# Kernel tuning notes

Measured on AMD Instinct MI355X. Metric: run time of the kernel, lower is better.

## Reference

```python
import jax, jax.numpy as jnp
import numpy as np

R_MAX = 5.0
P_CUT = 5
NAVG = 16.0
L_OF_LM = np.array([0, 1, 1, 1, 2, 2, 2, 2, 2, 3, 3, 3, 3, 3, 3, 3])


def _sph(v):
    # real spherical harmonics up to l=3 on normalized vectors, [E,16]
    n = jnp.sqrt(jnp.sum(v * v, -1, keepdims=True) + 1e-12)
    u = v / n
    x, y, z = u[..., 0], u[..., 1], u[..., 2]
    s3, s15, s5 = np.sqrt(3.0), np.sqrt(15.0), np.sqrt(5.0)
    s70, s105, s42, s7 = np.sqrt(70.0), np.sqrt(105.0), np.sqrt(42.0), np.sqrt(7.0)
    Y = [jnp.ones_like(x),
         s3 * x, s3 * y, s3 * z,
         s15 * x * y, s15 * y * z, 0.5 * s5 * (3 * z * z - 1.0), s15 * x * z, 0.5 * s15 * (x * x - y * y),
         0.25 * s70 * y * (3 * x * x - y * y), s105 * x * y * z, 0.25 * s42 * y * (5 * z * z - 1.0),
         0.5 * s7 * z * (5 * z * z - 3.0), 0.25 * s42 * x * (5 * z * z - 1.0),
         0.5 * s105 * z * (x * x - y * y), 0.25 * s70 * x * (3 * x * x - y * y)]
    return jnp.stack(Y, -1)


def _radial(r):
    # Bessel basis * smooth polynomial cutoff, r: [E] -> [E, 8]
    n = jnp.arange(1, 9, dtype=r.dtype)
    bess = np.sqrt(2.0 / R_MAX) * jnp.sin(n * np.pi * r[:, None] / R_MAX) / (r[:, None] + 1e-9)
    u = r / R_MAX
    p = float(P_CUT)
    f = 1.0 - 0.5 * (p + 1) * (p + 2) * u ** P_CUT + p * (p + 2) * u ** (P_CUT + 1) - 0.5 * p * (p + 1) * u ** (P_CUT + 2)
    f = jnp.where(u < 1.0, f, 0.0)
    return bess * f[:, None]


def _energy(node_attrs, positions, shifts, atomic_energies, W_embed, W_up, W_r1, W_r2, W_r3,
            W_lin, W_skip, U1, U2, U3, Wc1, Wc2, Wc3, W_prod, W_readout,
            edge_index, batch, num_graphs):
    send, recv = edge_index[0], edge_index[1]
    vec = positions[recv] - positions[send] + shifts
    r = jnp.sqrt(jnp.sum(vec * vec, -1) + 1e-12)
    Y = _sph(vec)                       # [E,16]
    edge_feats = _radial(r)             # [E,8]
    h = node_attrs @ W_embed            # [N,K] scalar node features
    lidx = jnp.asarray(L_OF_LM)
    N = h.shape[0]
    for i in range(2):
        h_up = h @ W_up[i]
        w = jax.nn.silu(edge_feats @ W_r1[i])
        w = jax.nn.silu(w @ W_r2[i])
        w = (w @ W_r3[i]).reshape(edge_feats.shape[0], -1, 4)   # [E,K,4] per-l radial tp weights
        w_lm = w[:, :, lidx]                                    # [E,K,16]
        m = w_lm * h_up[send][:, :, None] * Y[:, None, :]       # scalar x SH tensor product messages
        agg = jax.ops.segment_sum(m, recv, num_segments=N) / NAVG
        Wm = W_lin[i][lidx]                                     # [16,K,K] per-l linear
        mixed = jnp.einsum('nkm,mkh->nhm', agg, Wm)
        sc = jnp.einsum('nk,ne,ekh->nh', h, node_attrs, W_skip[i])  # element-wise skip tp -> scalars
        A = mixed.at[:, :, 0].add(sc)                           # [N,K,16] A-basis
        # ACE symmetric product basis (invariant outputs), element-dependent weights
        w1 = jnp.einsum('ne,epk->npk', node_attrs, Wc1[i])
        b1 = jnp.einsum('nkp,npk->nk', jnp.einsum('nka,ap->nkp', A, U1), w1)
        AA = jnp.einsum('nka,nkb->nkab', A, A)                  # [N,K,16,16]
        w2 = jnp.einsum('ne,epk->npk', node_attrs, Wc2[i])
        b2 = jnp.einsum('nkp,npk->nk', jnp.einsum('nkab,abp->nkp', AA, U2), w2)
        T3 = jnp.einsum('nkab,abcp->nkcp', AA, U3)              # [N,K,16,8]
        w3 = jnp.einsum('ne,epk->npk', node_attrs, Wc3[i])
        b3 = jnp.einsum('nkp,npk->nk', jnp.einsum('nkcp,nkc->nkp', T3, A), w3)
        h = (b1 + b2 + b3) @ W_prod[i]
    node_es = h @ W_readout                                     # [N]
    node_e0 = node_attrs @ atomic_energies
    e0 = jax.ops.segment_sum(node_e0, batch, num_segments=num_graphs)
    inter = jax.ops.segment_sum(node_es, batch, num_segments=num_graphs)
    return e0 + inter


def setup_inputs():
    key = jax.random.key(0)
    ks = jax.random.split(key, 24)
    N, E, K, NE, G, NB = 2048, 32768, 128, 10, 16, 8
    P1, P2, P3, L = 2, 4, 8, 16

    def rn(k, shape, fan):
        return jax.random.normal(k, shape, jnp.float32) / np.sqrt(fan)

    elem = jax.random.randint(ks[0], (N,), 0, NE)
    return {
        'node_attrs': jax.nn.one_hot(elem, NE, dtype=jnp.float32),
        'positions': jax.random.uniform(ks[1], (N, 3), jnp.float32) * 6.0,
        'shifts': jnp.zeros((E, 3), jnp.float32),
        'atomic_energies': jax.random.normal(ks[2], (NE,), jnp.float32),
        'W_embed': rn(ks[3], (NE, K), NE),
        'W_up': rn(ks[4], (2, K, K), K),
        'W_r1': rn(ks[5], (2, NB, 64), NB),
        'W_r2': rn(ks[6], (2, 64, 64), 64),
        'W_r3': rn(ks[7], (2, 64, K * 4), 64),
        'W_lin': rn(ks[8], (2, 4, K, K), K),
        'W_skip': rn(ks[9], (2, NE, K, K), K),
        'U1': rn(ks[10], (L, P1), L),
        'U2': rn(ks[11], (L, L, P2), L * L),
        'U3': rn(ks[12], (L, L, L, P3), L * L * L),
        'Wc1': rn(ks[13], (2, NE, P1, K), P1),
        'Wc2': rn(ks[14], (2, NE, P2, K), P2),
        'Wc3': rn(ks[15], (2, NE, P3, K), P3),
        'W_prod': rn(ks[16], (2, K, K), K),
        'W_readout': rn(ks[17], (K,), K),
        'edge_index': jax.random.randint(ks[18], (2, E), 0, N).astype(jnp.int32),
        'batch': jnp.sort(jax.random.randint(ks[19], (N,), 0, G)).astype(jnp.int32),
        'num_graphs': 16,
    }


def reference(node_attrs, positions, shifts, atomic_energies, W_embed, W_up, W_r1, W_r2, W_r3,
              W_lin, W_skip, U1, U2, U3, Wc1, Wc2, Wc3, W_prod, W_readout,
              edge_index, batch, num_graphs):
    e_fn = lambda pos: _energy(node_attrs, pos, shifts, atomic_energies, W_embed, W_up, W_r1, W_r2,
                               W_r3, W_lin, W_skip, U1, U2, U3, Wc1, Wc2, Wc3, W_prod, W_readout,
                               edge_index, batch, num_graphs)
    energy = e_fn(positions)
    forces = -jax.grad(lambda p: e_fn(p).sum())(positions)
    return energy, forces
```

## Files before the change

kernel.cpp:

```cpp
#include <hip/hip_runtime.h>
#include <math.h>

#define KCH 128
#define NELEM 10

__device__ __forceinline__ int lidxf(int m){ return (m==0)?0:((m<4)?1:((m<9)?2:3)); }
__device__ __forceinline__ float siluf(float z){ return z/(1.f+expf(-z)); }
__device__ __forceinline__ float dsiluf(float z){ float s=1.f/(1.f+expf(-z)); return s*(1.f+z*(1.f-s)); }

__global__ void k_zero(float* p, int n){
  int i = blockIdx.x*256 + threadIdx.x;
  if(i<n) p[i]=0.f;
}

__global__ void k_elem(const float* attrs, int* elem, int N){
  int n = blockIdx.x*256 + threadIdx.x;
  if(n>=N) return;
  int z=0;
  for(int e=0;e<NELEM;++e) if(attrs[n*NELEM+e] > 0.5f) z=e;
  elem[n]=z;
}

__global__ void k_h0(const float* Wemb, const int* elem, float* h0, int N){
  int i = blockIdx.x*256 + threadIdx.x;
  if(i>=N*KCH) return;
  int n = i>>7, k = i&127;
  h0[i] = Wemb[elem[n]*KCH + k];
}

__global__ void k_hist(const int* keys, int* cnt, int n){
  int i = blockIdx.x*256 + threadIdx.x;
  if(i<n) atomicAdd(&cnt[keys[i]],1);
}

__global__ void k_scan(const int* cnt, int* ptr, int n){
  __shared__ int part[257];
  int t = threadIdx.x;
  int csz = (n+255)/256;
  int lo = t*csz, hi = (t+1)*csz; if(hi>n) hi=n;
  int s=0;
  for(int i=lo;i<hi;++i) s+=cnt[i];
  part[t]=s; __syncthreads();
  if(t==0){ int acc=0; for(int i=0;i<256;++i){ int v=part[i]; part[i]=acc; acc+=v; } part[256]=acc; }
  __syncthreads();
  int acc = part[t];
  for(int i=lo;i<hi;++i){ ptr[i]=acc; acc+=cnt[i]; }
  if(t==255) ptr[n]=part[256];
}

__global__ void k_scatter(const int* keys, const int* ptr, int* cur, int* idx, int n){
  int i = blockIdx.x*256 + threadIdx.x;
  if(i>=n) return;
  int k = keys[i];
  int p = atomicAdd(&cur[k],1);
  idx[ptr[k]+p] = i;
}

__global__ void k_tb(const float* src, float* dst, int nmat){
  int i = blockIdx.x*256 + threadIdx.x;
  if(i >= nmat*16384) return;
  int mat = i>>14, rc = i&16383, r = rc>>7, c = rc&127;
  dst[mat*16384 + c*128 + r] = src[i];
}

__global__ void k_tr(const float* src, float* dst, int R, int C){
  int i = blockIdx.x*256 + threadIdx.x;
  if(i>=R*C) return;
  int r=i/C, c=i-r*C;
  dst[c*R+r]=src[i];
}

__global__ void k_symU2(const float* U2, float* U2s){
  int i = blockIdx.x*256 + threadIdx.x;
  if(i>=1024) return;
  int p = i&3, b = (i>>2)&15, a = (i>>6)&15;
  U2s[i] = U2[a*64+b*4+p] + U2[b*64+a*4+p];
}

__global__ void k_symU3(const float* U3, float* U3s){
  int i = blockIdx.x*256 + threadIdx.x;
  if(i>=32768) return;
  int p = i&7, c = (i>>3)&15, b = (i>>7)&15, a = (i>>11)&15;
  float s = U3[a*2048+b*128+c*8+p] + U3[a*2048+c*128+b*8+p]
          + U3[b*2048+a*128+c*8+p] + U3[b*2048+c*128+a*8+p]
          + U3[c*2048+a*128+b*8+p] + U3[c*2048+b*128+a*8+p];
  U3s[i] = s;
}

__global__ void k_C1(const float* U1, const float* Wc1l, float* C1){
  int i = blockIdx.x*256 + threadIdx.x;
  if(i>=NELEM*KCH*16) return;
  int a = i&15, c = (i>>4)&127, z = i>>11;
  float s=0;
  for(int p=0;p<2;++p) s += U1[a*2+p]*Wc1l[z*2*KCH + p*KCH + c];
  C1[i]=s;
}

__global__ void k_C2S(const float* U2s, const float* Wc2l, float* C2S){
  int i = blockIdx.x*256 + threadIdx.x;
  if(i>=NELEM*KCH*256) return;
  int ab = i&255, c = (i>>8)&127, z = i>>15;
  float s=0;
  for(int p=0;p<4;++p) s += U2s[ab*4+p]*Wc2l[z*4*KCH + p*KCH + c];
  C2S[i]=s;
}

__global__ void k_T(const float* U3s, const float* Wc3l, float* T){
  int i = blockIdx.x*256 + threadIdx.x;
  if(i>=NELEM*KCH*4096) return;
  int abc = i&4095, c = (i>>12)&127, z = i>>19;
  float s=0;
  for(int p=0;p<8;++p) s += U3s[abc*8+p]*Wc3l[z*8*KCH + p*KCH + c];
  T[i]=s;
}

__global__ void k_gB1(const float* Wro, const float* Wprod1, float* gB1){
  int c = threadIdx.x;
  float s=0;
  for(int h=0;h<KCH;++h) s += Wro[h]*Wprod1[c*KCH+h];
  gB1[c]=s;
}

__global__ void k_edge_geom(const float* pos, const float* shifts, const int* ei, int E,
                            float* vec, float* rr, float* Y, float* dY, float* ef, float* defdr){
  int e = blockIdx.x*256 + threadIdx.x;
  if(e>=E) return;
  int s = ei[e], rc = ei[E+e];
  float vx = pos[rc*3+0]-pos[s*3+0]+shifts[e*3+0];
  float vy = pos[rc*3+1]-pos[s*3+1]+shifts[e*3+1];
  float vz = pos[rc*3+2]-pos[s*3+2]+shifts[e*3+2];
  float r2 = vx*vx+vy*vy+vz*vz + 1e-12f;
  float n = sqrtf(r2);
  float inv_n = 1.f/n;
  float x = vx*inv_n, y = vy*inv_n, z = vz*inv_n;
  vec[e*3+0]=vx; vec[e*3+1]=vy; vec[e*3+2]=vz; rr[e]=n;
  const float s3=1.7320508075688772f, s15=3.8729833462074170f, s5=2.2360679774997896f;
  const float s70=8.3666002653407556f, s105=10.2469507659595980f, s42=6.4807406984078604f, s7=2.6457513110645907f;
  float Yv[16], d0[16], d1[16], d2[16];
  Yv[0]=1.f; d0[0]=0;d1[0]=0;d2[0]=0;
  Yv[1]=s3*x; d0[1]=s3; d1[1]=0; d2[1]=0;
  Yv[2]=s3*y; d0[2]=0; d1[2]=s3; d2[2]=0;
  Yv[3]=s3*z; d0[3]=0; d1[3]=0; d2[3]=s3;
  Yv[4]=s15*x*y; d0[4]=s15*y; d1[4]=s15*x; d2[4]=0;
  Yv[5]=s15*y*z; d0[5]=0; d1[5]=s15*z; d2[5]=s15*y;
  Yv[6]=0.5f*s5*(3.f*z*z-1.f); d0[6]=0; d1[6]=0; d2[6]=3.f*s5*z;
  Yv[7]=s15*x*z; d0[7]=s15*z; d1[7]=0; d2[7]=s15*x;
  Yv[8]=0.5f*s15*(x*x-y*y); d0[8]=s15*x; d1[8]=-s15*y; d2[8]=0;
  Yv[9]=0.25f*s70*y*(3.f*x*x-y*y); d0[9]=1.5f*s70*x*y; d1[9]=0.75f*s70*(x*x-y*y); d2[9]=0;
  Yv[10]=s105*x*y*z; d0[10]=s105*y*z; d1[10]=s105*x*z; d2[10]=s105*x*y;
  Yv[11]=0.25f*s42*y*(5.f*z*z-1.f); d0[11]=0; d1[11]=0.25f*s42*(5.f*z*z-1.f); d2[11]=2.5f*s42*y*z;
  Yv[12]=0.5f*s7*z*(5.f*z*z-3.f); d0[12]=0; d1[12]=0; d2[12]=0.5f*s7*(15.f*z*z-3.f);
  Yv[13]=0.25f*s42*x*(5.f*z*z-1.f); d0[13]=0.25f*s42*(5.f*z*z-1.f); d1[13]=0; d2[13]=2.5f*s42*x*z;
  Yv[14]=0.5f*s105*z*(x*x-y*y); d0[14]=s105*x*z; d1[14]=-s105*y*z; d2[14]=0.5f*s105*(x*x-y*y);
  Yv[15]=0.25f*s70*x*(3.f*x*x-y*y); d0[15]=0.25f*s70*(9.f*x*x-y*y); d1[15]=-0.5f*s70*x*y; d2[15]=0;
  #pragma unroll
  for(int m=0;m<16;++m){
    float dm = d0[m]*x + d1[m]*y + d2[m]*z;
    dY[(size_t)e*48 + m*3 + 0] = (d0[m]-dm*x)*inv_n;
    dY[(size_t)e*48 + m*3 + 1] = (d1[m]-dm*y)*inv_n;
    dY[(size_t)e*48 + m*3 + 2] = (d2[m]-dm*z)*inv_n;
    Y[(size_t)e*16+m] = Yv[m];
  }
  const float c0 = 0.63245553203367587f;
  float rp = n + 1e-9f;
  float u = n*0.2f;
  float f, dfdr;
  if(u < 1.f){
    float u2=u*u, u4=u2*u2, u5=u4*u, u6=u5*u, u7=u6*u;
    f = 1.f - 21.f*u5 + 35.f*u6 - 15.f*u7;
    float dfdu = -105.f*u4 + 210.f*u5 - 105.f*u6;
    dfdr = dfdu*0.2f;
  } else { f=0.f; dfdr=0.f; }
  for(int b=0;b<8;++b){
    float kn = (float)(b+1)*0.62831853071795865f;
    float sr = sinf(kn*n), cr = cosf(kn*n);
    float bess = c0*sr/rp;
    float dbess = c0*(kn*cr/rp - sr/(rp*rp));
    ef[(size_t)e*8+b] = bess*f;
    defdr[(size_t)e*8+b] = dbess*f + bess*dfdr;
  }
}

__global__ __launch_bounds__(128) void k_mm(const float* X, const float* W, float* Out, int N, int acc){
  __shared__ float xs[8][KCH];
  int t = threadIdx.x;
  int n0 = blockIdx.x*8;
  for(int j=0;j<8;++j){ int n=n0+j; xs[j][t] = (n<N)? X[(size_t)n*KCH+t] : 0.f; }
  __syncthreads();
  float a[8] = {0,0,0,0,0,0,0,0};
  for(int s=0;s<KCH;++s){
    float wv = W[s*KCH + t];
    #pragma unroll
    for(int j=0;j<8;++j) a[j] += xs[j][s]*wv;
  }
  for(int j=0;j<8;++j){
    int n=n0+j;
    if(n<N){ if(acc) Out[(size_t)n*KCH+t] += a[j]; else Out[(size_t)n*KCH+t] = a[j]; }
  }
}

__global__ __launch_bounds__(256) void k_radial_w(const float* ef, const float* Wr1, const float* Wr2, const float* Wr3,
                                                  float* w, int E){
  __shared__ float t1s[16][64];
  __shared__ float t2s[16][64];
  int t = threadIdx.x;
  int e0 = blockIdx.x*16;
  for(int it=0; it<4; ++it){
    int item = t + it*256;
    int el = item>>6, j = item&63;
    float z=0;
    if(e0+el < E){
      const float* efe = ef + (size_t)(e0+el)*8;
      #pragma unroll
      for(int b=0;b<8;++b) z += efe[b]*Wr1[b*64+j];
    }
    t1s[el][j] = siluf(z);
  }
  __syncthreads();
  for(int it=0; it<4; ++it){
    int item = t + it*256;
    int el = item>>6, j = item&63;
    float z=0;
    #pragma unroll
    for(int i=0;i<64;++i) z += t1s[el][i]*Wr2[i*64+j];
    t2s[el][j] = siluf(z);
  }
  __syncthreads();
  float a0[16], a1[16];
  #pragma unroll
  for(int el=0;el<16;++el){ a0[el]=0.f; a1[el]=0.f; }
  for(int j=0;j<64;++j){
    float wa = Wr3[j*512 + t];
    float wb = Wr3[j*512 + t + 256];
    #pragma unroll
    for(int el=0;el<16;++el){
      float tv = t2s[el][j];
      a0[el] += tv*wa;
      a1[el] += tv*wb;
    }
  }
  for(int el=0;el<16;++el){
    if(e0+el < E){
      w[(size_t)(e0+el)*512 + t] = a0[el];
      w[(size_t)(e0+el)*512 + t + 256] = a1[el];
    }
  }
}

__global__ __launch_bounds__(256) void k_gather(const float* hup, const float* w, const float* Y,
                                                const int* rptr, const int* ridx, const int* ei,
                                                float* agg, int E){
  int n = blockIdx.x;
  int t = threadIdx.x;
  int k = t & 127, mg = t >> 7;
  float acc[8] = {0,0,0,0,0,0,0,0};
  int s0 = rptr[n], s1 = rptr[n+1];
  for(int i=s0;i<s1;++i){
    int e = ridx[i];
    int snd = ei[e];
    float hv = hup[(size_t)snd*KCH + k];
    float4 w4 = ((const float4*)(w + (size_t)e*512))[k];
    const float* Ye = Y + (size_t)e*16 + mg*8;
    if(mg==0){
      acc[0] += w4.x*hv*Ye[0];
      acc[1] += w4.y*hv*Ye[1];
      acc[2] += w4.y*hv*Ye[2];
      acc[3] += w4.y*hv*Ye[3];
      acc[4] += w4.z*hv*Ye[4];
      acc[5] += w4.z*hv*Ye[5];
      acc[6] += w4.z*hv*Ye[6];
      acc[7] += w4.z*hv*Ye[7];
    } else {
      acc[0] += w4.z*hv*Ye[0];
      acc[1] += w4.w*hv*Ye[1];
      acc[2] += w4.w*hv*Ye[2];
      acc[3] += w4.w*hv*Ye[3];
      acc[4] += w4.w*hv*Ye[4];
      acc[5] += w4.w*hv*Ye[5];
      acc[6] += w4.w*hv*Ye[6];
      acc[7] += w4.w*hv*Ye[7];
    }
  }
  const float inv = 1.f/16.f;
  float* ap = agg + (size_t)n*2048 + k*16 + mg*8;
  #pragma unroll
  for(int j=0;j<8;++j) ap[j] = acc[j]*inv;
}

__global__ __launch_bounds__(128) void k_mixed(const float* X, const float* hin, const int* elem,
                                               const float* Wl4, const float* Wskip_l,
                                               float* Out, int N, int doskip){
  __shared__ float xs[8][KCH];
  __shared__ float hs[8][KCH];
  int t = threadIdx.x;
  int m = blockIdx.y;
  int n0 = blockIdx.x*8;
  for(int j=0;j<8;++j) xs[j][t] = X[(size_t)(n0+j)*2048 + t*16 + m];
  int l = lidxf(m);
  if(doskip && m==0) for(int j=0;j<8;++j) hs[j][t] = hin[(size_t)(n0+j)*KCH + t];
  __syncthreads();
  const float* W = Wl4 + l*KCH*KCH;
  float a[8]={0,0,0,0,0,0,0,0};
  for(int s=0;s<KCH;++s){
    float wv = W[s*KCH + t];
    #pragma unroll
    for(int j=0;j<8;++j) a[j] += xs[j][s]*wv;
  }
  if(doskip && m==0){
    int zs[8];
    for(int j=0;j<8;++j) zs[j]=elem[n0+j];
    for(int s=0;s<KCH;++s){
      #pragma unroll
      for(int j=0;j<8;++j) a[j] += hs[j][s]*Wskip_l[(size_t)zs[j]*KCH*KCH + s*KCH + t];
    }
  }
  for(int j=0;j<8;++j) Out[(size_t)(n0+j)*2048 + t*16 + m] = a[j];
}

__global__ __launch_bounds__(256) void k_poly_fwd(const float* A, const float* C1, const float* C2S, const float* T,
                                                  const int* eptr, const int* eidx, float* B){
  __shared__ float Ts[4096];
  __shared__ float C2s_[256];
  __shared__ float C1s_[16];
  int t = threadIdx.x;
  int z = blockIdx.x >> 7, c = blockIdx.x & 127;
  size_t cb = (size_t)z*KCH + c;
  for(int i=t;i<4096;i+=256) Ts[i] = T[cb*4096 + i];
  for(int i=t;i<256;i+=256) C2s_[i] = C2S[cb*256 + i];
  if(t<16) C1s_[t] = C1[cb*16 + t];
  __syncthreads();
  int s0 = eptr[z], cnt = eptr[z+1]-s0;
  for(int idx=t; idx<cnt; idx+=256){
    int n = eidx[s0+idx];
    float a[16];
    const float4* ap = (const float4*)(A + (size_t)n*2048 + c*16);
    float4 a4;
    a4=ap[0]; a[0]=a4.x;a[1]=a4.y;a[2]=a4.z;a[3]=a4.w;
    a4=ap[1]; a[4]=a4.x;a[5]=a4.y;a[6]=a4.z;a[7]=a4.w;
    a4=ap[2]; a[8]=a4.x;a[9]=a4.y;a[10]=a4.z;a[11]=a4.w;
    a4=ap[3]; a[12]=a4.x;a[13]=a4.y;a[14]=a4.z;a[15]=a4.w;
    float b1=0;
    #pragma unroll
    for(int i=0;i<16;++i) b1 += a[i]*C1s_[i];
    float b2=0;
    for(int i=0;i<16;++i){
      float s=0;
      #pragma unroll
      for(int j=0;j<16;++j) s += a[j]*C2s_[i*16+j];
      b2 += a[i]*s;
    }
    float b3=0;
    for(int i=0;i<16;++i){
      for(int j=0;j<16;++j){
        float p = a[i]*a[j];
        const float* Tp = &Ts[(i*16+j)*16];
        float s=0;
        #pragma unroll
        for(int kk=0;kk<16;++kk) s += Tp[kk]*a[kk];
        b3 += p*s;
      }
    }
    B[(size_t)n*KCH + c] = b1 + 0.5f*b2 + b3*(1.f/6.f);
  }
}

__global__ __launch_bounds__(256) void k_poly_bwd(const float* A, const float* C1, const float* C2S, const float* T,
                                                  const int* eptr, const int* eidx,
                                                  const float* gBvec, const float* gBbuf, float* gA){
  __shared__ float Ts[4096];
  __shared__ float C2s_[256];
  __shared__ float C1s_[16];
  int t = threadIdx.x;
  int z = blockIdx.x >> 7, c = blockIdx.x & 127;
  size_t cb = (size_t)z*KCH + c;
  for(int i=t;i<4096;i+=256) Ts[i] = T[cb*4096 + i];
  for(int i=t;i<256;i+=256) C2s_[i] = C2S[cb*256 + i];
  if(t<16) C1s_[t] = C1[cb*16 + t];
  __syncthreads();
  int s0 = eptr[z], cnt = eptr[z+1]-s0;
  for(int idx=t; idx<cnt; idx+=256){
    int n = eidx[s0+idx];
    float a[16];
    const float4* ap = (const float4*)(A + (size_t)n*2048 + c*16);
    float4 a4;
    a4=ap[0]; a[0]=a4.x;a[1]=a4.y;a[2]=a4.z;a[3]=a4.w;
    a4=ap[1]; a[4]=a4.x;a[5]=a4.y;a[6]=a4.z;a[7]=a4.w;
    a4=ap[2]; a[8]=a4.x;a[9]=a4.y;a[10]=a4.z;a[11]=a4.w;
    a4=ap[3]; a[12]=a4.x;a[13]=a4.y;a[14]=a4.z;a[15]=a4.w;
    float gB = gBvec ? gBvec[c] : gBbuf[(size_t)n*KCH + c];
    float g12[16], g3[16];
    #pragma unroll
    for(int x=0;x<16;++x){ g12[x]=C1s_[x]; g3[x]=0.f; }
    for(int x=0;x<16;++x){
      float s=0;
      #pragma unroll
      for(int b=0;b<16;++b) s += a[b]*C2s_[x*16+b];
      g12[x]+=s;
    }
    for(int b=0;b<16;++b){
      for(int c2=0;c2<16;++c2){
        float p = a[b]*a[c2];
        const float* Tp = &Ts[(b*16+c2)*16];
        #pragma unroll
        for(int x=0;x<16;++x) g3[x] += p*Tp[x];
      }
    }
    float* gp = gA + (size_t)n*2048 + c*16;
    #pragma unroll
    for(int x=0;x<16;++x) gp[x] = gB*(g12[x] + 0.5f*g3[x]);
  }
}

__global__ __launch_bounds__(128) void k_skip_bwd(const float* gA, const float* WskipT, const int* elem, float* gh){
  __shared__ float gs[KCH];
  int n = blockIdx.x, t = threadIdx.x;
  gs[t] = gA[(size_t)n*2048 + t*16];
  __syncthreads();
  int z = elem[n];
  const float* W = WskipT + (size_t)z*KCH*KCH;
  float acc=0;
  for(int h=0;h<KCH;++h) acc += gs[h]*W[h*KCH+t];
  gh[(size_t)n*KCH+t] += acc;
}

__global__ __launch_bounds__(256) void k_edge_bwd2(const float* gagg, const float* hup, const float* w,
                                                   const float* Y, const float* dY,
                                                   const float* vec, const float* rr,
                                                   const float* ef, const float* defdr,
                                                   const float* Wr1, const float* Wr2,
                                                   const float* Wr2T, const float* Wr3T,
                                                   const int* ei, int E,
                                                   float* ghup, float* gvec, int do_ghup){
  __shared__ float Ys[4][16];
  __shared__ float gwS[4][512];
  __shared__ float gYp[4][2][16];
  __shared__ float t1s[4][64];
  __shared__ float gz2s[4][64];
  __shared__ float efS[4][8];
  __shared__ float defS[4][8];
  int t = threadIdx.x;
  int e0 = blockIdx.x*4;
  const float inv16 = 1.f/16.f;
  if(t<64){ int le=t>>4; int ec = e0+le; if(ec<E) Ys[le][t&15] = Y[(size_t)ec*16 + (t&15)]; }
  else if(t<96){ int i=t-64; int le=i>>3; int ec=e0+le; if(ec<E) efS[le][i&7]=ef[(size_t)ec*8+(i&7)]; }
  else if(t<128){ int i=t-96; int le=i>>3; int ec=e0+le; if(ec<E) defS[le][i&7]=defdr[(size_t)ec*8+(i&7)]; }
  __syncthreads();
  for(int rep=0;rep<2;++rep){
    int le = (t>>7) + 2*rep;
    int k = t&127;
    int e = e0+le;
    bool valid = (e<E);
    int eC = valid ? e : (E-1);
    int snd = ei[eC], rcv = ei[E+eC];
    float hv = hup[(size_t)snd*KCH + k];
    float4 w4 = ((const float4*)(w + (size_t)eC*512))[k];
    float g[16];
    const float4* gp = (const float4*)(gagg + (size_t)rcv*2048 + k*16);
    float4 v4;
    v4=gp[0]; g[0]=v4.x;g[1]=v4.y;g[2]=v4.z;g[3]=v4.w;
    v4=gp[1]; g[4]=v4.x;g[5]=v4.y;g[6]=v4.z;g[7]=v4.w;
    v4=gp[2]; g[8]=v4.x;g[9]=v4.y;g[10]=v4.z;g[11]=v4.w;
    v4=gp[3]; g[12]=v4.x;g[13]=v4.y;g[14]=v4.z;g[15]=v4.w;
    const float* Yl = Ys[le];
    float p0 = g[0]*Yl[0];
    float p1 = g[1]*Yl[1]+g[2]*Yl[2]+g[3]*Yl[3];
    float p2 = g[4]*Yl[4]+g[5]*Yl[5]+g[6]*Yl[6]+g[7]*Yl[7]+g[8]*Yl[8];
    float p3 = g[9]*Yl[9]+g[10]*Yl[10]+g[11]*Yl[11]+g[12]*Yl[12]+g[13]*Yl[13]+g[14]*Yl[14]+g[15]*Yl[15];
    float hs = hv*inv16;
    ((float4*)(&gwS[le][k*4]))[0] = make_float4(p0*hs, p1*hs, p2*hs, p3*hs);
    if(do_ghup && valid){
      float s = (p0*w4.x + p1*w4.y + p2*w4.z + p3*w4.w)*inv16;
      atomicAdd(&ghup[(size_t)snd*KCH+k], s);
    }
    float q[16];
    q[0]=g[0]*w4.x*hv;
    q[1]=g[1]*w4.y*hv; q[2]=g[2]*w4.y*hv; q[3]=g[3]*w4.y*hv;
    q[4]=g[4]*w4.z*hv; q[5]=g[5]*w4.z*hv; q[6]=g[6]*w4.z*hv; q[7]=g[7]*w4.z*hv; q[8]=g[8]*w4.z*hv;
    #pragma unroll
    for(int m=9;m<16;++m) q[m]=g[m]*w4.w*hv;
    #pragma unroll
    for(int m=0;m<16;++m){
      float vv=q[m];
      #pragma unroll
      for(int off2=1; off2<64; off2<<=1) vv += __shfl_xor(vv, off2, 64);
      q[m]=vv;
    }
    if((t&63)==0){
      int wv2 = (t>>6)&1;
      #pragma unroll
      for(int m=0;m<16;++m) gYp[le][wv2][m]=q[m];
    }
  }
  __syncthreads();
  {
    int el = t>>6, j = t&63;
    int e = e0+el;
    bool valid = (e<E);
    int eC = valid ? e : (E-1);
    float z1=0;
    #pragma unroll
    for(int b=0;b<8;++b) z1 += efS[el][b]*Wr1[b*64+j];
    float ds1v = dsiluf(z1);
    t1s[el][j] = siluf(z1);
    __syncthreads();
    float z2=0;
    for(int i=0;i<64;++i) z2 += t1s[el][i]*Wr2[i*64+j];
    float ds2v = dsiluf(z2);
    float gt2=0;
    for(int i=0;i<512;++i) gt2 += gwS[el][i]*Wr3T[i*64+j];
    gz2s[el][j] = gt2*ds2v;
    __syncthreads();
    float gz1=0;
    for(int o=0;o<64;++o) gz1 += gz2s[el][o]*Wr2T[o*64+j];
    gz1 *= ds1v;
    float cj=0;
    #pragma unroll
    for(int b=0;b<8;++b) cj += Wr1[b*64+j]*defS[el][b];
    float p = gz1*cj;
    #pragma unroll
    for(int off2=1;off2<64;off2<<=1) p += __shfl_xor(p,off2,64);
    if(j<3 && valid){
      float s = p * vec[(size_t)eC*3+j] / rr[eC];
      #pragma unroll
      for(int m=0;m<16;++m)
        s += (gYp[el][0][m]+gYp[el][1][m])*inv16 * dY[(size_t)eC*48 + m*3 + j];
      gvec[(size_t)eC*3+j] += s;
    }
  }
}

__global__ void k_energy(const float* h2, const float* Wro, const float* AE,
                         const int* elem, const int* batch, float* out, int N){
  int n = blockIdx.x*256 + threadIdx.x;
  if(n>=N) return;
  float s=0;
  for(int k=0;k<KCH;++k) s += h2[(size_t)n*KCH+k]*Wro[k];
  s += AE[elem[n]];
  atomicAdd(&out[batch[n]], s);
}

__global__ void k_forces(const float* gvec, const int* ei, int E, float* fout){
  int i = blockIdx.x*256 + threadIdx.x;
  if(i>=E*3) return;
  int e = i/3, j = i - e*3;
  float g = gvec[i];
  atomicAdd(&fout[(size_t)ei[e]*3+j], g);
  atomicAdd(&fout[(size_t)ei[E+e]*3+j], -g);
}

extern "C" void kernel_launch(void* const* d_in, const int* in_sizes, int n_in,
                              void* d_out, int out_size, void* d_ws, size_t ws_size,
                              hipStream_t stream){
  const float* attrs  = (const float*)d_in[0];
  const float* pos    = (const float*)d_in[1];
  const float* shifts = (const float*)d_in[2];
  const float* AE     = (const float*)d_in[3];
  const float* Wemb   = (const float*)d_in[4];
  const float* Wup    = (const float*)d_in[5];
  const float* Wr1    = (const float*)d_in[6];
  const float* Wr2    = (const float*)d_in[7];
  const float* Wr3    = (const float*)d_in[8];
  const float* Wlin   = (const float*)d_in[9];
  const float* Wskip  = (const float*)d_in[10];
  const float* U1     = (const float*)d_in[11];
  const float* U2     = (const float*)d_in[12];
  const float* U3     = (const float*)d_in[13];
  const float* Wc1    = (const float*)d_in[14];
  const float* Wc2    = (const float*)d_in[15];
  const float* Wc3    = (const float*)d_in[16];
  const float* Wprod  = (const float*)d_in[17];
  const float* Wro    = (const float*)d_in[18];
  const int*   ei     = (const int*)d_in[19];
  const int*   batch  = (const int*)d_in[20];
  int N = in_sizes[1]/3;
  int E = in_sizes[19]/2;
  float* out = (float*)d_out;
  int G = out_size - 3*N;

  char* base = (char*)d_ws;
  size_t off = 0;
  auto alloc = [&](size_t nbytes)->void*{
    void* p = base + off;
    off += (nbytes + 255) & ~(size_t)255;
    return p;
  };
  int* elem = (int*)alloc((size_t)N*4);
  int* rptr = (int*)alloc((size_t)(N+1)*4);
  int* rcnt = (int*)alloc((size_t)N*4);
  int* rcur = (int*)alloc((size_t)N*4);
  int* ridx = (int*)alloc((size_t)E*4);
  int* eptr = (int*)alloc((size_t)(NELEM+1)*4);
  int* ecnt = (int*)alloc((size_t)NELEM*4);
  int* ecur = (int*)alloc((size_t)NELEM*4);
  int* eidx = (int*)alloc((size_t)N*4);
  float* h0   = (float*)alloc((size_t)N*KCH*4);
  float* h1   = (float*)alloc((size_t)N*KCH*4);
  float* h2   = (float*)alloc((size_t)N*KCH*4);
  float* hup0 = (float*)alloc((size_t)N*KCH*4);
  float* hup1 = (float*)alloc((size_t)N*KCH*4);
  float* vecb = (float*)alloc((size_t)E*3*4);
  float* rb   = (float*)alloc((size_t)E*4);
  float* Yb   = (float*)alloc((size_t)E*16*4);
  float* dYb  = (float*)alloc((size_t)E*48*4);
  float* efb  = (float*)alloc((size_t)E*8*4);
  float* defb = (float*)alloc((size_t)E*8*4);
  float* wb   = (float*)alloc((size_t)E*512*4);
  float* A0   = (float*)alloc((size_t)N*2048*4);
  float* A1   = (float*)alloc((size_t)N*2048*4);
  float* aggb = (float*)alloc((size_t)N*2048*4);
  float* gAb  = (float*)alloc((size_t)N*2048*4);
  float* Bbuf = (float*)alloc((size_t)N*KCH*4);
  float* gh1  = (float*)alloc((size_t)N*KCH*4);
  float* ghup = (float*)alloc((size_t)N*KCH*4);
  float* gB0b = (float*)alloc((size_t)N*KCH*4);
  float* gB1v = (float*)alloc((size_t)KCH*4);
  float* gvecb= (float*)alloc((size_t)E*3*4);
  float* C1b  = (float*)alloc((size_t)NELEM*KCH*16*4);
  float* C2Sb = (float*)alloc((size_t)NELEM*KCH*256*4);
  float* Tb   = (float*)alloc((size_t)NELEM*KCH*4096*4);
  float* U2s  = (float*)alloc(1024*4);
  float* U3s  = (float*)alloc(32768*4);
  float* WupT1   = (float*)alloc(16384*4);
  float* WprodT0 = (float*)alloc(16384*4);
  float* WskipT1 = (float*)alloc((size_t)NELEM*16384*4);
  float* WlinT   = (float*)alloc((size_t)8*16384*4);
  float* Wr3T0   = (float*)alloc(32768*4);
  float* Wr3T1   = (float*)alloc(32768*4);
  float* Wr2T0   = (float*)alloc(4096*4);
  float* Wr2T1   = (float*)alloc(4096*4);
  if(off > ws_size) return;
  float* wb1 = wb; int have_wb1 = 0;
  if(off + (size_t)E*512*4 <= ws_size){ wb1 = (float*)alloc((size_t)E*512*4); have_wb1 = 1; }

  const int KK = KCH*KCH;
  dim3 b256(256), b128(128);
  #define GR(n) dim3(((n)+255)/256)

  k_zero<<<GR(out_size),b256,0,stream>>>(out, out_size);
  k_zero<<<GR(N),b256,0,stream>>>((float*)rcnt, N);
  k_zero<<<GR(N),b256,0,stream>>>((float*)rcur, N);
  k_zero<<<GR(NELEM),b256,0,stream>>>((float*)ecnt, NELEM);
  k_zero<<<GR(NELEM),b256,0,stream>>>((float*)ecur, NELEM);
  k_zero<<<GR(N*KCH),b256,0,stream>>>(gh1, N*KCH);
  k_zero<<<GR(N*KCH),b256,0,stream>>>(ghup, N*KCH);
  k_zero<<<GR(E*3),b256,0,stream>>>(gvecb, E*3);

  k_elem<<<GR(N),b256,0,stream>>>(attrs, elem, N);
  k_h0<<<GR(N*KCH),b256,0,stream>>>(Wemb, elem, h0, N);

  k_hist<<<GR(E),b256,0,stream>>>(ei+E, rcnt, E);
  k_scan<<<1,b256,0,stream>>>(rcnt, rptr, N);
  k_scatter<<<GR(E),b256,0,stream>>>(ei+E, rptr, rcur, ridx, E);
  k_hist<<<GR(N),b256,0,stream>>>(elem, ecnt, N);
  k_scan<<<1,b256,0,stream>>>(ecnt, eptr, NELEM);
  k_scatter<<<GR(N),b256,0,stream>>>(elem, eptr, ecur, eidx, N);

  k_tb<<<GR(KK),b256,0,stream>>>(Wup + KK, WupT1, 1);
  k_tb<<<GR(KK),b256,0,stream>>>(Wprod, WprodT0, 1);
  k_tb<<<GR(NELEM*KK),b256,0,stream>>>(Wskip + (size_t)NELEM*KK, WskipT1, NELEM);
  k_tb<<<GR(8*KK),b256,0,stream>>>(Wlin, WlinT, 8);
  k_tr<<<GR(32768),b256,0,stream>>>(Wr3, Wr3T0, 64, 512);
  k_tr<<<GR(32768),b256,0,stream>>>(Wr3 + 32768, Wr3T1, 64, 512);
  k_tr<<<GR(4096),b256,0,stream>>>(Wr2, Wr2T0, 64, 64);
  k_tr<<<GR(4096),b256,0,stream>>>(Wr2 + 4096, Wr2T1, 64, 64);

  k_symU2<<<GR(1024),b256,0,stream>>>(U2, U2s);
  k_symU3<<<GR(32768),b256,0,stream>>>(U3, U3s);
  k_gB1<<<1,b128,0,stream>>>(Wro, Wprod + KK, gB1v);

  k_edge_geom<<<GR(E),b256,0,stream>>>(pos, shifts, ei, E, vecb, rb, Yb, dYb, efb, defb);

  dim3 mmG((N+7)/8);
  dim3 mixG((N+7)/8, 16);
  dim3 polyG(NELEM*KCH);
  dim3 rwG((E+15)/16);
  dim3 ebG((E+3)/4);

  k_C1 <<<GR(NELEM*KCH*16),  b256,0,stream>>>(U1,  Wc1, C1b);
  k_C2S<<<GR(NELEM*KCH*256), b256,0,stream>>>(U2s, Wc2, C2Sb);
  k_T  <<<GR(NELEM*KCH*4096),b256,0,stream>>>(U3s, Wc3, Tb);
  k_mm<<<mmG,b128,0,stream>>>(h0, Wup, hup0, N, 0);
  k_radial_w<<<rwG,b256,0,stream>>>(efb, Wr1, Wr2, Wr3, wb, E);
  k_gather<<<dim3(N),b256,0,stream>>>(hup0, wb, Yb, rptr, ridx, ei, aggb, E);
  k_mixed<<<mixG,b128,0,stream>>>(aggb, h0, elem, Wlin, Wskip, A0, N, 1);
  k_poly_fwd<<<polyG,b256,0,stream>>>(A0, C1b, C2Sb, Tb, eptr, eidx, Bbuf);
  k_mm<<<mmG,b128,0,stream>>>(Bbuf, Wprod, h1, N, 0);

  k_C1 <<<GR(NELEM*KCH*16),  b256,0,stream>>>(U1,  Wc1 + NELEM*2*KCH, C1b);
  k_C2S<<<GR(NELEM*KCH*256), b256,0,stream>>>(U2s, Wc2 + NELEM*4*KCH, C2Sb);
  k_T  <<<GR(NELEM*KCH*4096),b256,0,stream>>>(U3s, Wc3 + NELEM*8*KCH, Tb);
  k_mm<<<mmG,b128,0,stream>>>(h1, Wup + KK, hup1, N, 0);
  k_radial_w<<<rwG,b256,0,stream>>>(efb, Wr1 + 512, Wr2 + 4096, Wr3 + 32768, wb1, E);
  k_gather<<<dim3(N),b256,0,stream>>>(hup1, wb1, Yb, rptr, ridx, ei, aggb, E);
  k_mixed<<<mixG,b128,0,stream>>>(aggb, h1, elem, Wlin + 4*KK, Wskip + (size_t)NELEM*KK, A1, N, 1);
  k_poly_fwd<<<polyG,b256,0,stream>>>(A1, C1b, C2Sb, Tb, eptr, eidx, Bbuf);
  k_mm<<<mmG,b128,0,stream>>>(Bbuf, Wprod + KK, h2, N, 0);

  k_energy<<<GR(N),b256,0,stream>>>(h2, Wro, AE, elem, batch, out, N);

  k_poly_bwd<<<polyG,b256,0,stream>>>(A1, C1b, C2Sb, Tb, eptr, eidx, gB1v, nullptr, gAb);
  k_mixed<<<mixG,b128,0,stream>>>(gAb, nullptr, elem, WlinT + 4*KK, nullptr, aggb, N, 0);
  k_skip_bwd<<<dim3(N),b128,0,stream>>>(gAb, WskipT1, elem, gh1);
  k_edge_bwd2<<<ebG,b256,0,stream>>>(aggb, hup1, wb1, Yb, dYb, vecb, rb, efb, defb,
                                     Wr1 + 512, Wr2 + 4096, Wr2T1, Wr3T1, ei, E, ghup, gvecb, 1);
  k_mm<<<mmG,b128,0,stream>>>(ghup, WupT1, gh1, N, 1);

  k_C1 <<<GR(NELEM*KCH*16),  b256,0,stream>>>(U1,  Wc1, C1b);
  k_C2S<<<GR(NELEM*KCH*256), b256,0,stream>>>(U2s, Wc2, C2Sb);
  k_T  <<<GR(NELEM*KCH*4096),b256,0,stream>>>(U3s, Wc3, Tb);
  k_mm<<<mmG,b128,0,stream>>>(gh1, WprodT0, gB0b, N, 0);
  k_poly_bwd<<<polyG,b256,0,stream>>>(A0, C1b, C2Sb, Tb, eptr, eidx, nullptr, gB0b, gAb);
  k_mixed<<<mixG,b128,0,stream>>>(gAb, nullptr, elem, WlinT, nullptr, aggb, N, 0);
  if(!have_wb1)
    k_radial_w<<<rwG,b256,0,stream>>>(efb, Wr1, Wr2, Wr3, wb, E);
  k_edge_bwd2<<<ebG,b256,0,stream>>>(aggb, hup0, wb, Yb, dYb, vecb, rb, efb, defb,
                                     Wr1, Wr2, Wr2T0, Wr3T0, ei, E, ghup, gvecb, 0);

  k_forces<<<GR(E*3),b256,0,stream>>>(gvecb, ei, E, out + G);
  #undef GR
}
```

Before: 1.852 ms.

## Sort edges by receiver, fuse mixed-linear and skip kernels, cache layer-1 coupling tensors

Edge geometry, the radial weights and the edge backward now run in receiver-sorted edge order, with sender and receiver indices stored per sorted slot. This removes the ridx/ei indirection in the gather and makes its per-edge reads contiguous. The per-m mixed-linear kernel is replaced by a register-tiled kernel that expands Wlin to per-m weight matrices, uses vectorised float4 loads, and folds the skip-connection matmul (forward and backward) into the same launch, which removes k_skip_bwd and two zeroing kernels. When workspace allows, the layer-1 C1/C2S/T tensors are kept in separate buffers so the layer-0 tensors need not be recomputed in the backward pass, at the cost of extra memory and larger expanded weight buffers.

```diff
diff --git a/kernel.cpp b/kernel.cpp
--- a/kernel.cpp
+++ b/kernel.cpp
@@ -70,6 +70,19 @@
   dst[c*R+r]=src[i];
 }
 
+__global__ void k_wbig(const float* Wl4, float* Wb){
+  int i = blockIdx.x*256 + threadIdx.x;
+  if(i>=16*16384) return;
+  int m = i>>14, sk = i&16383;
+  Wb[i] = Wl4[lidxf(m)*16384 + sk];
+}
+__global__ void k_wbigT(const float* Wl4, float* Wb){
+  int i = blockIdx.x*256 + threadIdx.x;
+  if(i>=16*16384) return;
+  int m = i>>14, sk = i&16383, s = sk>>7, k = sk&127;
+  Wb[i] = Wl4[lidxf(m)*16384 + k*128 + s];
+}
+
 __global__ void k_symU2(const float* U2, float* U2s){
   int i = blockIdx.x*256 + threadIdx.x;
   if(i>=1024) return;
@@ -121,11 +134,14 @@
   gB1[c]=s;
 }
 
-__global__ void k_edge_geom(const float* pos, const float* shifts, const int* ei, int E,
+__global__ void k_edge_geom(const float* pos, const float* shifts, const int* ei, const int* ridx, int E,
+                            int* snds, int* rcvs,
                             float* vec, float* rr, float* Y, float* dY, float* ef, float* defdr){
-  int e = blockIdx.x*256 + threadIdx.x;
-  if(e>=E) return;
+  int i = blockIdx.x*256 + threadIdx.x;
+  if(i>=E) return;
+  int e = ridx[i];
   int s = ei[e], rc = ei[E+e];
+  snds[i]=s; rcvs[i]=rc;
   float vx = pos[rc*3+0]-pos[s*3+0]+shifts[e*3+0];
   float vy = pos[rc*3+1]-pos[s*3+1]+shifts[e*3+1];
   float vz = pos[rc*3+2]-pos[s*3+2]+shifts[e*3+2];
@@ -133,7 +149,7 @@
   float n = sqrtf(r2);
   float inv_n = 1.f/n;
   float x = vx*inv_n, y = vy*inv_n, z = vz*inv_n;
-  vec[e*3+0]=vx; vec[e*3+1]=vy; vec[e*3+2]=vz; rr[e]=n;
+  vec[i*3+0]=vx; vec[i*3+1]=vy; vec[i*3+2]=vz; rr[i]=n;
   const float s3=1.7320508075688772f, s15=3.8729833462074170f, s5=2.2360679774997896f;
   const float s70=8.3666002653407556f, s105=10.2469507659595980f, s42=6.4807406984078604f, s7=2.6457513110645907f;
   float Yv[16], d0[16], d1[16], d2[16];
@@ -156,10 +172,10 @@
   #pragma unroll
   for(int m=0;m<16;++m){
     float dm = d0[m]*x + d1[m]*y + d2[m]*z;
-    dY[(size_t)e*48 + m*3 + 0] = (d0[m]-dm*x)*inv_n;
-    dY[(size_t)e*48 + m*3 + 1] = (d1[m]-dm*y)*inv_n;
-    dY[(size_t)e*48 + m*3 + 2] = (d2[m]-dm*z)*inv_n;
-    Y[(size_t)e*16+m] = Yv[m];
+    dY[(size_t)i*48 + m*3 + 0] = (d0[m]-dm*x)*inv_n;
+    dY[(size_t)i*48 + m*3 + 1] = (d1[m]-dm*y)*inv_n;
+    dY[(size_t)i*48 + m*3 + 2] = (d2[m]-dm*z)*inv_n;
+    Y[(size_t)i*16+m] = Yv[m];
   }
   const float c0 = 0.63245553203367587f;
   float rp = n + 1e-9f;
@@ -176,8 +192,8 @@
     float sr = sinf(kn*n), cr = cosf(kn*n);
     float bess = c0*sr/rp;
     float dbess = c0*(kn*cr/rp - sr/(rp*rp));
-    ef[(size_t)e*8+b] = bess*f;
-    defdr[(size_t)e*8+b] = dbess*f + bess*dfdr;
+    ef[(size_t)i*8+b] = bess*f;
+    defdr[(size_t)i*8+b] = dbess*f + bess*dfdr;
   }
 }
 
@@ -248,7 +264,7 @@
 }
 
 __global__ __launch_bounds__(256) void k_gather(const float* hup, const float* w, const float* Y,
-                                                const int* rptr, const int* ridx, const int* ei,
+                                                const int* rptr, const int* snds,
                                                 float* agg, int E){
   int n = blockIdx.x;
   int t = threadIdx.x;
@@ -256,11 +272,10 @@
   float acc[8] = {0,0,0,0,0,0,0,0};
   int s0 = rptr[n], s1 = rptr[n+1];
   for(int i=s0;i<s1;++i){
-    int e = ridx[i];
-    int snd = ei[e];
+    int snd = snds[i];
     float hv = hup[(size_t)snd*KCH + k];
-    float4 w4 = ((const float4*)(w + (size_t)e*512))[k];
-    const float* Ye = Y + (size_t)e*16 + mg*8;
+    float4 w4 = ((const float4*)(w + (size_t)i*512))[k];
+    const float* Ye = Y + (size_t)i*16 + mg*8;
     if(mg==0){
       acc[0] += w4.x*hv*Ye[0];
       acc[1] += w4.y*hv*Ye[1];
@@ -287,34 +302,75 @@
   for(int j=0;j<8;++j) ap[j] = acc[j]*inv;
 }
 
-__global__ __launch_bounds__(128) void k_mixed(const float* X, const float* hin, const int* elem,
-                                               const float* Wl4, const float* Wskip_l,
-                                               float* Out, int N, int doskip){
-  __shared__ float xs[8][KCH];
-  __shared__ float hs[8][KCH];
+__global__ __launch_bounds__(256) void k_mixed2(const float* X, const float* hin, const int* elem,
+                                                const float* Wb, const float* Wsk,
+                                                float* Out, float* gh, int N, int mode){
+  __shared__ float xs[4][2048];
+  __shared__ float hs[4][128];
+  __shared__ int zs[4];
   int t = threadIdx.x;
-  int m = blockIdx.y;
-  int n0 = blockIdx.x*8;
-  for(int j=0;j<8;++j) xs[j][t] = X[(size_t)(n0+j)*2048 + t*16 + m];
-  int l = lidxf(m);
-  if(doskip && m==0) for(int j=0;j<8;++j) hs[j][t] = hin[(size_t)(n0+j)*KCH + t];
-  __syncthreads();
-  const float* W = Wl4 + l*KCH*KCH;
-  float a[8]={0,0,0,0,0,0,0,0};
+  int n0 = blockIdx.x*4;
+  for(int q=0;q<4;++q){
+    const float4* Xp = (const float4*)(X + (size_t)(n0+q)*2048);
+    float4* Xs = (float4*)xs[q];
+    Xs[t] = Xp[t]; Xs[t+256] = Xp[t+256];
+  }
+  if(mode==0 && t<128){
+    for(int q=0;q<4;++q) hs[q][t] = hin[(size_t)(n0+q)*KCH + t];
+  }
+  if(t<4) zs[t]=elem[n0+t];
+  __syncthreads();
+  int kg = t&31, mg=(t>>5)&3, half=t>>7;
+  int k0 = kg*4, m0 = mg*4;
+  int q0 = half*2, q1=q0+1;
+  float acc0[4][4], acc1[4][4];
+  #pragma unroll
+  for(int a=0;a<4;++a){
+    #pragma unroll
+    for(int b=0;b<4;++b){acc0[a][b]=0.f;acc1[a][b]=0.f;}
+  }
   for(int s=0;s<KCH;++s){
-    float wv = W[s*KCH + t];
-    #pragma unroll
-    for(int j=0;j<8;++j) a[j] += xs[j][s]*wv;
-  }
-  if(doskip && m==0){
-    int zs[8];
-    for(int j=0;j<8;++j) zs[j]=elem[n0+j];
+    float4 x0 = *(const float4*)&xs[q0][s*16+m0];
+    float4 x1 = *(const float4*)&xs[q1][s*16+m0];
+    #pragma unroll
+    for(int mj=0;mj<4;++mj){
+      const float4 wv = *(const float4*)&Wb[(size_t)(m0+mj)*16384 + s*128 + k0];
+      float xm0 = (mj==0)?x0.x:((mj==1)?x0.y:((mj==2)?x0.z:x0.w));
+      float xm1 = (mj==0)?x1.x:((mj==1)?x1.y:((mj==2)?x1.z:x1.w));
+      acc0[mj][0]+=xm0*wv.x; acc0[mj][1]+=xm0*wv.y; acc0[mj][2]+=xm0*wv.z; acc0[mj][3]+=xm0*wv.w;
+      acc1[mj][0]+=xm1*wv.x; acc1[mj][1]+=xm1*wv.y; acc1[mj][2]+=xm1*wv.z; acc1[mj][3]+=xm1*wv.w;
+    }
+  }
+  if(mode==0 && mg==0){
+    const float* W0 = Wsk + (size_t)zs[q0]*16384;
+    const float* W1 = Wsk + (size_t)zs[q1]*16384;
     for(int s=0;s<KCH;++s){
-      #pragma unroll
-      for(int j=0;j<8;++j) a[j] += hs[j][s]*Wskip_l[(size_t)zs[j]*KCH*KCH + s*KCH + t];
-    }
-  }
-  for(int j=0;j<8;++j) Out[(size_t)(n0+j)*2048 + t*16 + m] = a[j];
+      float h0v=hs[q0][s], h1v=hs[q1][s];
+      float4 w0 = *(const float4*)&W0[s*128+k0];
+      float4 w1 = *(const float4*)&W1[s*128+k0];
+      acc0[0][0]+=h0v*w0.x; acc0[0][1]+=h0v*w0.y; acc0[0][2]+=h0v*w0.z; acc0[0][3]+=h0v*w0.w;
+      acc1[0][0]+=h1v*w1.x; acc1[0][1]+=h1v*w1.y; acc1[0][2]+=h1v*w1.z; acc1[0][3]+=h1v*w1.w;
+    }
+  }
+  #pragma unroll
+  for(int ki=0;ki<4;++ki){
+    *(float4*)&Out[(size_t)(n0+q0)*2048 + (k0+ki)*16 + m0] = make_float4(acc0[0][ki],acc0[1][ki],acc0[2][ki],acc0[3][ki]);
+    *(float4*)&Out[(size_t)(n0+q1)*2048 + (k0+ki)*16 + m0] = make_float4(acc1[0][ki],acc1[1][ki],acc1[2][ki],acc1[3][ki]);
+  }
+  if(mode==2 && mg==0){
+    const float* W0 = Wsk + (size_t)zs[q0]*16384;
+    const float* W1 = Wsk + (size_t)zs[q1]*16384;
+    float a0[4]={0,0,0,0}, a1[4]={0,0,0,0};
+    for(int s=0;s<KCH;++s){
+      float x0v = xs[q0][s*16], x1v = xs[q1][s*16];
+      float4 w0 = *(const float4*)&W0[s*128+k0];
+      float4 w1 = *(const float4*)&W1[s*128+k0];
+      a0[0]+=x0v*w0.x; a0[1]+=x0v*w0.y; a0[2]+=x0v*w0.z; a0[3]+=x0v*w0.w;
+      a1[0]+=x1v*w1.x; a1[1]+=x1v*w1.y; a1[2]+=x1v*w1.z; a1[3]+=x1v*w1.w;
+    }
+    *(float4*)&gh[(size_t)(n0+q0)*KCH + k0] = make_float4(a0[0],a0[1],a0[2],a0[3]);
+    *(float4*)&gh[(size_t)(n0+q1)*KCH + k0] = make_float4(a1[0],a1[1],a1[2],a1[3]);
+  }
 }
 
 __global__ __launch_bounds__(256) void k_poly_fwd(const float* A, const float* C1, const float* C2S, const float* T,
@@ -411,26 +467,14 @@
   }
 }
 
-__global__ __launch_bounds__(128) void k_skip_bwd(const float* gA, const float* WskipT, const int* elem, float* gh){
-  __shared__ float gs[KCH];
-  int n = blockIdx.x, t = threadIdx.x;
-  gs[t] = gA[(size_t)n*2048 + t*16];
-  __syncthreads();
-  int z = elem[n];
-  const float* W = WskipT + (size_t)z*KCH*KCH;
-  float acc=0;
-  for(int h=0;h<KCH;++h) acc += gs[h]*W[h*KCH+t];
-  gh[(size_t)n*KCH+t] += acc;
-}
-
 __global__ __launch_bounds__(256) void k_edge_bwd2(const float* gagg, const float* hup, const float* w,
                                                    const float* Y, const float* dY,
                                                    const float* vec, const float* rr,
                                                    const float* ef, const float* defdr,
                                                    const float* Wr1, const float* Wr2,
                                                    const float* Wr2T, const float* Wr3T,
-                                                   const int* ei, int E,
-                                                   float* ghup, float* gvec, int do_ghup){
+                                                   const int* snds, const int* rcvs, int E,
+                                                   float* ghup, float* gvec, int do_ghup, int accv){
   __shared__ float Ys[4][16];
   __shared__ float gwS[4][512];
   __shared__ float gYp[4][2][16];
@@ -451,7 +495,7 @@
     int e = e0+le;
     bool valid = (e<E);
     int eC = valid ? e : (E-1);
-    int snd = ei[eC], rcv = ei[E+eC];
+    int snd = snds[eC], rcv = rcvs[eC];
     float hv = hup[(size_t)snd*KCH + k];
     float4 w4 = ((const float4*)(w + (size_t)eC*512))[k];
     float g[16];
@@ -524,7 +568,8 @@
       #pragma unroll
       for(int m=0;m<16;++m)
         s += (gYp[el][0][m]+gYp[el][1][m])*inv16 * dY[(size_t)eC*48 + m*3 + j];
-      gvec[(size_t)eC*3+j] += s;
+      if(accv) gvec[(size_t)eC*3+j] += s;
+      else     gvec[(size_t)eC*3+j]  = s;
     }
   }
 }
@@ -539,13 +584,13 @@
   atomicAdd(&out[batch[n]], s);
 }
 
-__global__ void k_forces(const float* gvec, const int* ei, int E, float* fout){
+__global__ void k_forces(const float* gvec, const int* snds, const int* rcvs, int E, float* fout){
   int i = blockIdx.x*256 + threadIdx.x;
   if(i>=E*3) return;
   int e = i/3, j = i - e*3;
   float g = gvec[i];
-  atomicAdd(&fout[(size_t)ei[e]*3+j], g);
-  atomicAdd(&fout[(size_t)ei[E+e]*3+j], -g);
+  atomicAdd(&fout[(size_t)snds[e]*3+j], g);
+  atomicAdd(&fout[(size_t)rcvs[e]*3+j], -g);
 }
 
 extern "C" void kernel_launch(void* const* d_in, const int* in_sizes, int n_in,
@@ -593,6 +638,8 @@
   int* ecnt = (int*)alloc((size_t)NELEM*4);
   int* ecur = (int*)alloc((size_t)NELEM*4);
   int* eidx = (int*)alloc((size_t)N*4);
+  int* snds = (int*)alloc((size_t)E*4);
+  int* rcvs = (int*)alloc((size_t)E*4);
   float* h0   = (float*)alloc((size_t)N*KCH*4);
   float* h1   = (float*)alloc((size_t)N*KCH*4);
   float* h2   = (float*)alloc((size_t)N*KCH*4);
@@ -623,7 +670,10 @@
   float* WupT1   = (float*)alloc(16384*4);
   float* WprodT0 = (float*)alloc(16384*4);
   float* WskipT1 = (float*)alloc((size_t)NELEM*16384*4);
-  float* WlinT   = (float*)alloc((size_t)8*16384*4);
+  float* Wbig0  = (float*)alloc((size_t)16*16384*4);
+  float* Wbig1  = (float*)alloc((size_t)16*16384*4);
+  float* WbigT0 = (float*)alloc((size_t)16*16384*4);
+  float* WbigT1 = (float*)alloc((size_t)16*16384*4);
   float* Wr3T0   = (float*)alloc(32768*4);
   float* Wr3T1   = (float*)alloc(32768*4);
   float* Wr2T0   = (float*)alloc(4096*4);
@@ -631,6 +681,16 @@
   if(off > ws_size) return;
   float* wb1 = wb; int have_wb1 = 0;
   if(off + (size_t)E*512*4 <= ws_size){ wb1 = (float*)alloc((size_t)E*512*4); have_wb1 = 1; }
+  float *C1_1=C1b, *C2_1=C2Sb, *T_1=Tb; int have_c2 = 0;
+  {
+    size_t need = ((size_t)NELEM*KCH*16 + (size_t)NELEM*KCH*256 + (size_t)NELEM*KCH*4096)*4 + 1024;
+    if(off + need <= ws_size){
+      C1_1 = (float*)alloc((size_t)NELEM*KCH*16*4);
+      C2_1 = (float*)alloc((size_t)NELEM*KCH*256*4);
+      T_1  = (float*)alloc((size_t)NELEM*KCH*4096*4);
+      have_c2 = 1;
+    }
+  }
 
   const int KK = KCH*KCH;
   dim3 b256(256), b128(128);
@@ -641,9 +701,7 @@
   k_zero<<<GR(N),b256,0,stream>>>((float*)rcur, N);
   k_zero<<<GR(NELEM),b256,0,stream>>>((float*)ecnt, NELEM);
   k_zero<<<GR(NELEM),b256,0,stream>>>((float*)ecur, NELEM);
-  k_zero<<<GR(N*KCH),b256,0,stream>>>(gh1, N*KCH);
   k_zero<<<GR(N*KCH),b256,0,stream>>>(ghup, N*KCH);
-  k_zero<<<GR(E*3),b256,0,stream>>>(gvecb, E*3);
 
   k_elem<<<GR(N),b256,0,stream>>>(attrs, elem, N);
   k_h0<<<GR(N*KCH),b256,0,stream>>>(Wemb, elem, h0, N);
@@ -658,7 +716,10 @@
   k_tb<<<GR(KK),b256,0,stream>>>(Wup + KK, WupT1, 1);
   k_tb<<<GR(KK),b256,0,stream>>>(Wprod, WprodT0, 1);
   k_tb<<<GR(NELEM*KK),b256,0,stream>>>(Wskip + (size_t)NELEM*KK, WskipT1, NELEM);
-  k_tb<<<GR(8*KK),b256,0,stream>>>(Wlin, WlinT, 8);
+  k_wbig <<<GR(16*KK),b256,0,stream>>>(Wlin, Wbig0);
+  k_wbig <<<GR(16*KK),b256,0,stream>>>(Wlin + 4*KK, Wbig1);
+  k_wbigT<<<GR(16*KK),b256,0,stream>>>(Wlin, WbigT0);
+  k_wbigT<<<GR(16*KK),b256,0,stream>>>(Wlin + 4*KK, WbigT1);
   k_tr<<<GR(32768),b256,0,stream>>>(Wr3, Wr3T0, 64, 512);
   k_tr<<<GR(32768),b256,0,stream>>>(Wr3 + 32768, Wr3T1, 64, 512);
   k_tr<<<GR(4096),b256,0,stream>>>(Wr2, Wr2T0, 64, 64);
@@ -668,10 +729,11 @@
   k_symU3<<<GR(32768),b256,0,stream>>>(U3, U3s);
   k_gB1<<<1,b128,0,stream>>>(Wro, Wprod + KK, gB1v);
 
-  k_edge_geom<<<GR(E),b256,0,stream>>>(pos, shifts, ei, E, vecb, rb, Yb, dYb, efb, defb);
+  k_edge_geom<<<GR(E),b256,0,stream>>>(pos, shifts, ei, ridx, E, snds, rcvs,
+                                       vecb, rb, Yb, dYb, efb, defb);
 
   dim3 mmG((N+7)/8);
-  dim3 mixG((N+7)/8, 16);
+  dim3 mxG((N+3)/4);
   dim3 polyG(NELEM*KCH);
   dim3 rwG((E+15)/16);
   dim3 ebG((E+3)/4);
@@ -681,41 +743,44 @@
   k_T  <<<GR(NELEM*KCH*4096),b256,0,stream>>>(U3s, Wc3, Tb);
   k_mm<<<mmG,b128,0,stream>>>(h0, Wup, hup0, N, 0);
   k_radial_w<<<rwG,b256,0,stream>>>(efb, Wr1, Wr2, Wr3, wb, E);
-  k_gather<<<dim3(N),b256,0,stream>>>(hup0, wb, Yb, rptr, ridx, ei, aggb, E);
-  k_mixed<<<mixG,b128,0,stream>>>(aggb, h0, elem, Wlin, Wskip, A0, N, 1);
+  k_gather<<<dim3(N),b256,0,stream>>>(hup0, wb, Yb, rptr, snds, aggb, E);
+  k_mixed2<<<mxG,b256,0,stream>>>(aggb, h0, elem, Wbig0, Wskip, A0, nullptr, N, 0);
   k_poly_fwd<<<polyG,b256,0,stream>>>(A0, C1b, C2Sb, Tb, eptr, eidx, Bbuf);
   k_mm<<<mmG,b128,0,stream>>>(Bbuf, Wprod, h1, N, 0);
 
-  k_C1 <<<GR(NELEM*KCH*16),  b256,0,stream>>>(U1,  Wc1 + NELEM*2*KCH, C1b);
-  k_C2S<<<GR(NELEM*KCH*256), b256,0,stream>>>(U2s, Wc2 + NELEM*4*KCH, C2Sb);
-  k_T  <<<GR(NELEM*KCH*4096),b256,0,stream>>>(U3s, Wc3 + NELEM*8*KCH, Tb);
+  k_C1 <<<GR(NELEM*KCH*16),  b256,0,stream>>>(U1,  Wc1 + NELEM*2*KCH, C1_1);
+  k_C2S<<<GR(NELEM*KCH*256), b256,0,stream>>>(U2s, Wc2 + NELEM*4*KCH, C2_1);
+  k_T  <<<GR(NELEM*KCH*4096),b256,0,stream>>>(U3s, Wc3 + NELEM*8*KCH, T_1);
   k_mm<<<mmG,b128,0,stream>>>(h1, Wup + KK, hup1, N, 0);
   k_radial_w<<<rwG,b256,0,stream>>>(efb, Wr1 + 512, Wr2 + 4096, Wr3 + 32768, wb1, E);
-  k_gather<<<dim3(N),b256,0,stream>>>(hup1, wb1, Yb, rptr, ridx, ei, aggb, E);
-  k_mixed<<<mixG,b128,0,stream>>>(aggb, h1, elem, Wlin + 4*KK, Wskip + (size_t)NELEM*KK, A1, N, 1);
-  k_poly_fwd<<<polyG,b256,0,stream>>>(A1, C1b, C2Sb, Tb, eptr, eidx, Bbuf);
+  k_gather<<<dim3(N),b256,0,stream>>>(hup1, wb1, Yb, rptr, snds, aggb, E);
+  k_mixed2<<<mxG,b256,0,stream>>>(aggb, h1, elem, Wbig1, Wskip + (size_t)NELEM*KK, A1, nullptr, N, 0);
+  k_poly_fwd<<<polyG,b256,0,stream>>>(A1, C1_1, C2_1, T_1, eptr, eidx, Bbuf);
   k_mm<<<mmG,b128,0,stream>>>(Bbuf, Wprod + KK, h2, N, 0);
 
   k_energy<<<GR(N),b256,0,stream>>>(h2, Wro, AE, elem, batch, out, N);
 
-  k_poly_bwd<<<polyG,b256,0,stream>>>(A1, C1b, C2Sb, Tb, eptr, eidx, gB1v, nullptr, gAb);
-  k_mixed<<<mixG,b128,0,stream>>>(gAb, nullptr, elem, WlinT + 4*KK, nullptr, aggb, N, 0);
-  k_skip_bwd<<<dim3(N),b128,0,stream>>>(gAb, WskipT1, elem, gh1);
+  k_poly_bwd<<<polyG,b256,0,stream>>>(A1, C1_1, C2_1, T_1, eptr, eidx, gB1v, nullptr, gAb);
+  k_mixed2<<<mxG,b256,0,stream>>>(gAb, nullptr, elem, WbigT1, WskipT1, aggb, gh1, N, 2);
   k_edge_bwd2<<<ebG,b256,0,stream>>>(aggb, hup1, wb1, Yb, dYb, vecb, rb, efb, defb,
-                                     Wr1 + 512, Wr2 + 4096, Wr2T1, Wr3T1, ei, E, ghup, gvecb, 1);
+                                     Wr1 + 512, Wr2 + 4096, Wr2T1, Wr3T1, snds, rcvs, E,
+                                     ghup, gvecb, 1, 0);
   k_mm<<<mmG,b128,0,stream>>>(ghup, WupT1, gh1, N, 1);
 
-  k_C1 <<<GR(NELEM*KCH*16),  b256,0,stream>>>(U1,  Wc1, C1b);
-  k_C2S<<<GR(NELEM*KCH*256), b256,0,stream>>>(U2s, Wc2, C2Sb);
-  k_T  <<<GR(NELEM*KCH*4096),b256,0,stream>>>(U3s, Wc3, Tb);
+  if(!have_c2){
+    k_C1 <<<GR(NELEM*KCH*16),  b256,0,stream>>>(U1,  Wc1, C1b);
+    k_C2S<<<GR(NELEM*KCH*256), b256,0,stream>>>(U2s, Wc2, C2Sb);
+    k_T  <<<GR(NELEM*KCH*4096),b256,0,stream>>>(U3s, Wc3, Tb);
+  }
   k_mm<<<mmG,b128,0,stream>>>(gh1, WprodT0, gB0b, N, 0);
   k_poly_bwd<<<polyG,b256,0,stream>>>(A0, C1b, C2Sb, Tb, eptr, eidx, nullptr, gB0b, gAb);
-  k_mixed<<<mixG,b128,0,stream>>>(gAb, nullptr, elem, WlinT, nullptr, aggb, N, 0);
+  k_mixed2<<<mxG,b256,0,stream>>>(gAb, nullptr, elem, WbigT0, nullptr, aggb, nullptr, N, 1);
   if(!have_wb1)
     k_radial_w<<<rwG,b256,0,stream>>>(efb, Wr1, Wr2, Wr3, wb, E);
   k_edge_bwd2<<<ebG,b256,0,stream>>>(aggb, hup0, wb, Yb, dYb, vecb, rb, efb, defb,
-                                     Wr1, Wr2, Wr2T0, Wr3T0, ei, E, ghup, gvecb, 0);
-
-  k_forces<<<GR(E*3),b256,0,stream>>>(gvecb, ei, E, out + G);
+                                     Wr1, Wr2, Wr2T0, Wr3T0, snds, rcvs, E,
+                                     ghup, gvecb, 0, 1);
+
+  k_forces<<<GR(E*3),b256,0,stream>>>(gvecb, snds, rcvs, E, out + G);
   #undef GR
 }
```

Measured after the change: 1.866 ms. Within noise of the previous version (+0.8%).
